# Kernel optimization log

Hardware: AMD Instinct MI355X
Metric: run time of the kernel (lower is better)

## Reference

```python
import jax, jax.numpy as jnp
import numpy as np
import math

H = 8        # num_heads
DK = 64      # key_dim
DV = 64      # value_dim
FACTOR = 4


def setup_inputs() -> dict:
    key = jax.random.key(0)
    B, T, S, D = 4, 2048, 2048, 512
    Dout = H * DV
    ks = jax.random.split(key, 16)
    sample_k = min(int(FACTOR * math.log(S)), S)  # = 33
    inp = {
        "x_q": jax.random.normal(ks[0], (B, T, D), jnp.float32),
        "x_k": jax.random.normal(ks[1], (B, S, D), jnp.float32),
        "x_v": jax.random.normal(ks[2], (B, S, D), jnp.float32),
        "Wq": jax.random.normal(ks[3], (D, H * DK), jnp.float32) * 0.02,
        "bq": jnp.zeros((H * DK,), jnp.float32),
        "Wk": jax.random.normal(ks[4], (D, H * DK), jnp.float32) * 0.02,
        "bk": jnp.zeros((H * DK,), jnp.float32),
        "Wv": jax.random.normal(ks[5], (D, H * DV), jnp.float32) * 0.02,
        "bv": jnp.zeros((H * DV,), jnp.float32),
        "Wo": jax.random.normal(ks[6], (H * DV, Dout), jnp.float32) * 0.02,
        "bo": jnp.zeros((Dout,), jnp.float32),
        "index_sample": jax.random.randint(ks[7], (T, sample_k), 0, S, jnp.int32),
    }
    return inp


def reference(x_q, x_k, x_v, Wq, bq, Wk, bk, Wv, bv, Wo, bo, index_sample):
    B, T, D = x_q.shape
    S = x_k.shape[1]
    u = min(int(FACTOR * math.log(T)), T)  # n_top queries kept

    q = (x_q @ Wq + bq).reshape(B, T, H, DK)
    k = (x_k @ Wk + bk).reshape(B, S, H, DK)
    v = (x_v @ Wv + bv).reshape(B, S, H, DV)

    # --- _prob_QK: sampled QK to score queries ---
    ks = k[:, index_sample]                                  # [B,T,J,H,dk]
    qk_s = jnp.einsum('bthd,btjhd->bthj', q, ks)             # [B,T,H,J]
    M = qk_s.max(-1) - qk_s.mean(-1)                         # [B,T,H]
    _, top = jax.lax.top_k(jnp.transpose(M, (0, 2, 1)), u)   # [B,H,u]

    b_idx = jnp.arange(B)[:, None, None]
    h_idx = jnp.arange(H)[None, :, None]
    q_red = q[b_idx, top, h_idx]                             # [B,H,u,dk]
    qk = jnp.einsum('bhud,bshd->bhus', q_red, k)             # [B,H,u,S]

    # --- s0: default (no mask) context = mean of values over S ---
    ctx = jnp.broadcast_to(v.mean(axis=1, keepdims=True), (B, T, H, DV))
    ctx = jnp.transpose(ctx, (0, 2, 1, 3))                   # [B,H,T,dv]

    # --- s1: scaled softmax over full keys for top queries ---
    scores = jax.nn.softmax(qk * (1.0 / math.sqrt(DK)), axis=-1)
    attn = jnp.einsum('bhus,bshd->bhud', scores, v)          # [B,H,u,dv]

    # --- scatter top-query results into context / scores ---
    ctx = ctx.at[b_idx, h_idx, top].set(attn)                # [B,H,T,dv]
    final_scores = jnp.full((B, H, T, S), 1.0 / S, dtype=scores.dtype)
    final_scores = final_scores.at[b_idx, h_idx, top].set(scores)

    out = jnp.transpose(ctx, (0, 2, 1, 3)).reshape(B, T, H * DV)
    out = out @ Wo + bo                                      # [B,T,output_dim]
    return out, final_scores
```

## Files before the change

kernel.cpp:

```cpp
#include <hip/hip_runtime.h>

typedef __attribute__((ext_vector_type(8))) short short8;
typedef __attribute__((ext_vector_type(4))) float f32x4;

constexpr int Bn  = 4;
constexpr int Tn  = 2048;
constexpr int Sn  = 2048;
constexpr int Dn  = 512;
constexpr int Hn  = 8;
constexpr int DKn = 64;
constexpr int DVn = 64;
constexpr int HDn = 512;
constexpr int SKn = 30;
constexpr int Un  = 30;
constexpr int Gu  = 6;
constexpr int NGroups = Un / Gu;
constexpr int NAttnG  = Bn * Hn * NGroups;
constexpr int NOutF   = (Bn * Tn) / 8;
constexpr int RowSplit = 57344;
constexpr int NGemm  = 768;
constexpr int NFillA = RowSplit / 4;
constexpr int NTailF = (Bn * Hn * Tn - RowSplit) / 4;
constexpr float kScale = 0.125f;

constexpr int NWsplit = 192;
constexpr int NXsplit = 1536;
constexpr int NVPart  = 64;

__device__ __forceinline__ ushort bf16_rne(float x) {
  unsigned u = __float_as_uint(x);
  return (ushort)((u + 0x7fffu + ((u >> 16) & 1u)) >> 16);
}
__device__ __forceinline__ float bf16f(ushort h) {
  return __uint_as_float(((unsigned)h) << 16);
}

#define MFMA(accv, av, bv) \
  asm volatile("v_mfma_f32_16x16x32_bf16 %0, %1, %2, %0" : "+v"(accv) : "v"(av), "v"(bv))

__global__ __launch_bounds__(256) void prep_split_kernel(
    const float* __restrict__ xq, const float* __restrict__ xk, const float* __restrict__ xv,
    const float* __restrict__ Wq, const float* __restrict__ Wk, const float* __restrict__ Wv,
    ushort* __restrict__ XH, ushort* __restrict__ XL,
    ushort* __restrict__ WtH, ushort* __restrict__ WtL) {
  const int tid = threadIdx.x;
  const int bid = blockIdx.x;

  if (bid < NWsplit) {
    const int z = bid / 64, t = bid % 64;
    const int k0 = (t >> 3) * 64, n0 = (t & 7) * 64;
    const float* W = (z == 0) ? Wq : (z == 1) ? Wk : Wv;
    __shared__ float tile[64][65];
    const int r = tid >> 2, c0 = (tid & 3) * 16;
#pragma unroll
    for (int i = 0; i < 16; i += 4) {
      const float4 vv = *(const float4*)(W + (size_t)(k0 + r) * HDn + n0 + c0 + i);
      tile[r][c0 + i] = vv.x; tile[r][c0 + i + 1] = vv.y;
      tile[r][c0 + i + 2] = vv.z; tile[r][c0 + i + 3] = vv.w;
    }
    __syncthreads();
    unsigned hp[8], lp[8];
#pragma unroll
    for (int i = 0; i < 16; i += 2) {
      const float x0 = tile[c0 + i][r];
      const float x1 = tile[c0 + i + 1][r];
      const ushort h0 = bf16_rne(x0), h1 = bf16_rne(x1);
      const ushort l0 = bf16_rne(x0 - bf16f(h0)), l1 = bf16_rne(x1 - bf16f(h1));
      hp[i >> 1] = (unsigned)h0 | ((unsigned)h1 << 16);
      lp[i >> 1] = (unsigned)l0 | ((unsigned)l1 << 16);
    }
    const size_t off = (size_t)(z * 512 + n0 + r) * 512 + k0 + c0;
    *(uint4*)(WtH + off)     = make_uint4(hp[0], hp[1], hp[2], hp[3]);
    *(uint4*)(WtH + off + 8) = make_uint4(hp[4], hp[5], hp[6], hp[7]);
    *(uint4*)(WtL + off)     = make_uint4(lp[0], lp[1], lp[2], lp[3]);
    *(uint4*)(WtL + off + 8) = make_uint4(lp[4], lp[5], lp[6], lp[7]);
    return;
  }

  const int xb = bid - NWsplit;
  const int z = xb >> 9, blk = xb & 511;
  const float* X = (z == 0) ? xq : (z == 1) ? xk : xv;
  const size_t base = (size_t)blk * 8192;
  const float4* X4 = (const float4*)(X + base);
  ushort* oh = XH + (size_t)z * 8192 * 512 + base;
  ushort* ol = XL + (size_t)z * 8192 * 512 + base;
#pragma unroll
  for (int i = 0; i < 8; ++i) {
    const int e = i * 256 + tid;
    const float4 x = X4[e];
    const ushort h0 = bf16_rne(x.x), h1 = bf16_rne(x.y);
    const ushort h2 = bf16_rne(x.z), h3 = bf16_rne(x.w);
    const ushort l0 = bf16_rne(x.x - bf16f(h0)), l1 = bf16_rne(x.y - bf16f(h1));
    const ushort l2 = bf16_rne(x.z - bf16f(h2)), l3 = bf16_rne(x.w - bf16f(h3));
    *(uint2*)(oh + (size_t)e * 4) =
        make_uint2((unsigned)h0 | ((unsigned)h1 << 16), (unsigned)h2 | ((unsigned)h3 << 16));
    *(uint2*)(ol + (size_t)e * 4) =
        make_uint2((unsigned)l0 | ((unsigned)l1 << 16), (unsigned)l2 | ((unsigned)l3 << 16));
  }
}

__global__ __launch_bounds__(256, 2) void gemm_fill_kernel(
    const ushort* __restrict__ XH, const ushort* __restrict__ XL,
    const ushort* __restrict__ WtH, const ushort* __restrict__ WtL,
    const float* __restrict__ bq, const float* __restrict__ bk, const float* __restrict__ bv,
    float* __restrict__ qo, float* __restrict__ ko, float* __restrict__ vo,
    float* __restrict__ fscores) {
  const int bid = blockIdx.x;
  const int tid = threadIdx.x;

  if (bid >= NGemm) {
    const size_t r0 = (size_t)(bid - NGemm) * 4;
    const float c = 1.0f / Sn;
    const float4 c4v = make_float4(c, c, c, c);
    float4* fs4 = (float4*)fscores + r0 * (Sn / 4);
#pragma unroll
    for (int i = 0; i < 8; ++i) fs4[i * 256 + tid] = c4v;
    return;
  }

  __shared__ ushort AsH[128][40];
  __shared__ ushort AsL[128][40];
  __shared__ ushort BsH[128][40];
  __shared__ ushort BsL[128][40];

  const int z = bid >> 8;
  const int rem = bid & 255;
  const int bn = (rem & 3) * 128;
  const int bm = (rem >> 2) * 128;
  const float* bias = (z == 0) ? bq : (z == 1) ? bk : bv;
  float* Y = (z == 0) ? qo : (z == 1) ? ko : vo;

  const int lane = tid & 63;
  const int wave = tid >> 6;
  const int wm = wave >> 1, wn = wave & 1;
  const int fr = lane & 15;
  const int kg = (lane >> 4) * 8;

  const int sr = tid >> 1;
  const int sh = (tid & 1) * 16;
  const ushort* xh = XH + (size_t)(z * 8192 + bm + sr) * 512 + sh;
  const ushort* xl = XL + (size_t)(z * 8192 + bm + sr) * 512 + sh;
  const ushort* wh = WtH + (size_t)(z * 512 + bn + sr) * 512 + sh;
  const ushort* wl = WtL + (size_t)(z * 512 + bn + sr) * 512 + sh;

  f32x4 acc[4][4];
#pragma unroll
  for (int m = 0; m < 4; ++m)
#pragma unroll
    for (int n = 0; n < 4; ++n)
#pragma unroll
      for (int j = 0; j < 4; ++j) acc[m][n][j] = 0.f;

  uint4 st[8];
#define STG_LOAD(k0_) do { \
    st[0] = *(const uint4*)(xh + (k0_)); st[1] = *(const uint4*)(xh + (k0_) + 8); \
    st[2] = *(const uint4*)(xl + (k0_)); st[3] = *(const uint4*)(xl + (k0_) + 8); \
    st[4] = *(const uint4*)(wh + (k0_)); st[5] = *(const uint4*)(wh + (k0_) + 8); \
    st[6] = *(const uint4*)(wl + (k0_)); st[7] = *(const uint4*)(wl + (k0_) + 8); } while (0)

  STG_LOAD(0);
  for (int k0 = 0; k0 < Dn; k0 += 32) {
    __syncthreads();
    *(uint4*)&AsH[sr][sh] = st[0]; *(uint4*)&AsH[sr][sh + 8] = st[1];
    *(uint4*)&AsL[sr][sh] = st[2]; *(uint4*)&AsL[sr][sh + 8] = st[3];
    *(uint4*)&BsH[sr][sh] = st[4]; *(uint4*)&BsH[sr][sh + 8] = st[5];
    *(uint4*)&BsL[sr][sh] = st[6]; *(uint4*)&BsL[sr][sh + 8] = st[7];
    __syncthreads();
    if (k0 + 32 < Dn) STG_LOAD(k0 + 32);

    short8 aH[4], aL[4], bH[4], bL[4];
#pragma unroll
    for (int m = 0; m < 4; ++m) {
      aH[m] = *(const short8*)&AsH[wm * 64 + m * 16 + fr][kg];
      aL[m] = *(const short8*)&AsL[wm * 64 + m * 16 + fr][kg];
    }
#pragma unroll
    for (int n = 0; n < 4; ++n) {
      bH[n] = *(const short8*)&BsH[wn * 64 + n * 16 + fr][kg];
      bL[n] = *(const short8*)&BsL[wn * 64 + n * 16 + fr][kg];
    }
#pragma unroll
    for (int m = 0; m < 4; ++m)
#pragma unroll
      for (int n = 0; n < 4; ++n) {
        MFMA(acc[m][n], aH[m], bH[n]);
        MFMA(acc[m][n], aH[m], bL[n]);
        MFMA(acc[m][n], aL[m], bH[n]);
      }
  }
  asm volatile("s_nop 7\n\ts_nop 7");

  float bsv[4];
#pragma unroll
  for (int n = 0; n < 4; ++n) bsv[n] = bias[bn + wn * 64 + n * 16 + fr];
  const int rbase = bm + wm * 64 + (lane >> 4) * 4;
#pragma unroll
  for (int m = 0; m < 4; ++m) {
#pragma unroll
    for (int n = 0; n < 4; ++n) {
      const int col = bn + wn * 64 + n * 16 + fr;
#pragma unroll
      for (int j = 0; j < 4; ++j) {
        Y[(size_t)(rbase + m * 16 + j) * HDn + col] = acc[m][n][j] + bsv[n];
      }
    }
  }
#undef STG_LOAD
}

__global__ __launch_bounds__(64) void sampled_m_kernel(
    const float* __restrict__ q, const float* __restrict__ k,
    const int* __restrict__ idxs, float* __restrict__ Mt,
    const float* __restrict__ v, float* __restrict__ vpart) {
  if (blockIdx.x >= Bn * Tn) {
    const int pb = blockIdx.x - Bn * Tn;
    const int b = pb >> 4, part = pb & 15;
    const int ln = threadIdx.x;
    const float4* v4 = (const float4*)(v + (size_t)b * Sn * HDn);
    float4 a0 = make_float4(0.f, 0.f, 0.f, 0.f);
    float4 a1 = make_float4(0.f, 0.f, 0.f, 0.f);
    const int s0 = part * 128;
    for (int s = s0; s < s0 + 128; ++s) {
      const float4 x0 = v4[(size_t)s * 128 + ln * 2];
      const float4 x1 = v4[(size_t)s * 128 + ln * 2 + 1];
      a0.x += x0.x; a0.y += x0.y; a0.z += x0.z; a0.w += x0.w;
      a1.x += x1.x; a1.y += x1.y; a1.z += x1.z; a1.w += x1.w;
    }
    float4* vp4 = (float4*)vpart + (size_t)pb * 128;
    vp4[ln * 2] = a0; vp4[ln * 2 + 1] = a1;
    return;
  }

  const int bt = blockIdx.x;
  const int b = bt >> 11, t = bt & (Tn - 1);
  const int lane = threadIdx.x;
  const int jq = lane >> 4;
  const int d16 = lane & 15;
  __shared__ int sidx[32];
  if (lane < SKn) sidx[lane] = idxs[t * SKn + lane];
  if (lane >= SKn && lane < 32) sidx[lane] = 0;
  __syncthreads();
  const float* qrow = q + (size_t)bt * HDn;
  const float* kb = k + (size_t)b * Sn * HDn;
  for (int h = 0; h < Hn; ++h) {
    const float4 qv = *(const float4*)(qrow + h * DKn + d16 * 4);
    float mx = -1e30f, sum = 0.f;
#pragma unroll
    for (int jb = 0; jb < 32; jb += 4) {
      const int j = jb + jq;
      const int srow = sidx[j];
      const float4 kv = *(const float4*)(kb + (size_t)srow * HDn + h * DKn + d16 * 4);
      float p = kv.x * qv.x + kv.y * qv.y + kv.z * qv.z + kv.w * qv.w;
      p += __shfl_xor(p, 1);
      p += __shfl_xor(p, 2);
      p += __shfl_xor(p, 4);
      p += __shfl_xor(p, 8);
      if (j < SKn) { mx = fmaxf(mx, p); sum += p; }
    }
    mx = fmaxf(mx, __shfl_xor(mx, 16));
    mx = fmaxf(mx, __shfl_xor(mx, 32));
    sum += __shfl_xor(sum, 16);
    sum += __shfl_xor(sum, 32);
    if (lane == 0) Mt[((size_t)(b * Hn + h)) * Tn + t] = mx - sum * (1.0f / SKn);
  }
}

__global__ __launch_bounds__(256) void topk_vmean_base_kernel(
    const float* __restrict__ Mt, const float* __restrict__ vpart,
    const float* __restrict__ Wo, const float* __restrict__ bo,
    int* __restrict__ top, float* __restrict__ vmean, float* __restrict__ basep) {
  const int tid = threadIdx.x;
  const int lane = tid & 63, w = tid >> 6;
  __shared__ float vals[Tn];
  __shared__ float wv[4];
  __shared__ int wi[4];
  __shared__ float4 part[256];
  __shared__ float vm[HDn];

  if (blockIdx.x < 32) {
    const int bh = blockIdx.x;
    for (int i = tid; i < Tn; i += 256) vals[i] = Mt[(size_t)bh * Tn + i];
    __syncthreads();
    for (int u = 0; u < Un; ++u) {
      float bv = -1e30f; int bi = 0x7fffffff;
      for (int i = tid; i < Tn; i += 256) {
        const float x = vals[i];
        if (x > bv) { bv = x; bi = i; }
      }
#pragma unroll
      for (int o = 1; o < 64; o <<= 1) {
        const float ov = __shfl_xor(bv, o);
        const int oi = __shfl_xor(bi, o);
        if (ov > bv || (ov == bv && oi < bi)) { bv = ov; bi = oi; }
      }
      if (lane == 0) { wv[w] = bv; wi[w] = bi; }
      __syncthreads();
      bv = wv[0]; bi = wi[0];
#pragma unroll
      for (int j = 1; j < 4; ++j) {
        if (wv[j] > bv || (wv[j] == bv && wi[j] < bi)) { bv = wv[j]; bi = wi[j]; }
      }
      if (tid == 0) { top[bh * Un + u] = bi; vals[bi] = -1e30f; }
      __syncthreads();
    }
  } else {
    const int b = blockIdx.x - 32;
    const int c4 = tid & 127, half = tid >> 7;
    float4 acc = make_float4(0.f, 0.f, 0.f, 0.f);
    for (int p = half * 8; p < half * 8 + 8; ++p) {
      const float4 x = ((const float4*)vpart)[(size_t)(b * 16 + p) * 128 + c4];
      acc.x += x.x; acc.y += x.y; acc.z += x.z; acc.w += x.w;
    }
    part[tid] = acc;
    __syncthreads();
    if (half == 0) {
      float4 a = part[c4], bpp = part[128 + c4];
      const float sc = 1.0f / Sn;
      float4 r = make_float4((a.x + bpp.x) * sc, (a.y + bpp.y) * sc,
                             (a.z + bpp.z) * sc, (a.w + bpp.w) * sc);
      *(float4*)(vm + c4 * 4) = r;
      *(float4*)(vmean + b * HDn + c4 * 4) = r;
    }
    __syncthreads();
    const float4* Wo4 = (const float4*)Wo;
    float4 acc2 = make_float4(0.f, 0.f, 0.f, 0.f);
    for (int c = half * 256; c < half * 256 + 256; ++c) {
      const float vmc = vm[c];
      const float4 wrow = Wo4[(size_t)c * 128 + c4];
      acc2.x += vmc * wrow.x; acc2.y += vmc * wrow.y;
      acc2.z += vmc * wrow.z; acc2.w += vmc * wrow.w;
    }
    __syncthreads();
    part[tid] = acc2;
    __syncthreads();
    if (half == 0) {
      float4 a = part[c4], bpp = part[128 + c4];
      const float4 bb = ((const float4*)bo)[c4];
      float4 r = make_float4(a.x + bpp.x + bb.x, a.y + bpp.y + bb.y,
                             a.z + bpp.z + bb.z, a.w + bpp.w + bb.w);
      ((float4*)basep)[b * 128 + c4] = r;
    }
  }
}

__global__ __launch_bounds__(256) void attn_out_kernel(
    const float* __restrict__ q, const float* __restrict__ k,
    const float* __restrict__ v, const float* __restrict__ vmean,
    const int* __restrict__ top, const float* __restrict__ Wo,
    const float* __restrict__ basep,
    float* __restrict__ out, float* __restrict__ fscores) {
  const int tid = threadIdx.x;
  const int bid = blockIdx.x;

  if (bid >= NAttnG + NOutF) {
    const int fid = bid - NAttnG - NOutF;
    const int r = RowSplit + fid * 4;
    const int bh = r >> 11;
    const int tbase = r & (Tn - 1);
    __shared__ int sflag4[4];
    if (tid < 4) sflag4[tid] = 0;
    __syncthreads();
    if (tid < Un) {
      const int d = top[bh * Un + tid] - tbase;
      if (d >= 0 && d < 4) sflag4[d] = 1;
    }
    __syncthreads();
    const float c = 1.0f / Sn;
    const float4 c4v = make_float4(c, c, c, c);
    float4* fs4 = (float4*)fscores + (size_t)r * (Sn / 4);
#pragma unroll
    for (int rr = 0; rr < 4; ++rr) {
      if (!sflag4[rr]) {
        float4* row = fs4 + rr * (Sn / 4);
        row[tid] = c4v;
        row[256 + tid] = c4v;
      }
    }
    return;
  }

  if (bid >= NAttnG) {
    const int fid = bid - NAttnG;
    const int r0 = fid * 8;
    const int b = r0 >> 11;
    const int t0 = r0 & (Tn - 1);
    __shared__ int sflag8[8];
    if (tid < 8) sflag8[tid] = 0;
    __syncthreads();
    if (tid < Hn * Un) {
      const int d = top[b * Hn * Un + tid] - t0;
      if (d >= 0 && d < 8) sflag8[d] = 1;
    }
    __syncthreads();
    const int col4 = tid & 127, rh = tid >> 7;
    const float4 bv4 = ((const float4*)basep)[b * 128 + col4];
#pragma unroll
    for (int rp = 0; rp < 4; ++rp) {
      const int rr = rp * 2 + rh;
      float4* orow4 = (float4*)(out + (size_t)(r0 + rr) * HDn) + col4;
      if (sflag8[rr]) {
        float* p = (float*)orow4;
        atomicAdd(p + 0, bv4.x); atomicAdd(p + 1, bv4.y);
        atomicAdd(p + 2, bv4.z); atomicAdd(p + 3, bv4.w);
      } else {
        *orow4 = bv4;
      }
    }
    return;
  }

  const int grp = bid % NGroups;
  const int bh = bid / NGroups;
  const int h = bh & (Hn - 1), b = bh >> 3;
  const int u0 = grp * Gu;
  const int lane = tid & 63, w = tid >> 6;

  __shared__ float qs[Gu][DKn];
  __shared__ float sc[Gu][2052];
  __shared__ float red[8];
  __shared__ int tsel[Gu];
  __shared__ float4 partv[4][Gu][16];

  if (tid < Gu) tsel[tid] = top[bh * Un + u0 + tid];
  __syncthreads();
  for (int i = tid; i < Gu * DKn; i += 256) {
    const int g = i >> 6, d = i & 63;
    qs[g][d] = q[((size_t)(b * Tn + tsel[g])) * HDn + h * DKn + d];
  }
  __syncthreads();

  const float4* k4 = (const float4*)k;
  for (int s = tid; s < Sn; s += 256) {
    const float4* krow = k4 + ((size_t)(b * Sn + s)) * 128 + h * 16;
    float acc[Gu];
#pragma unroll
    for (int g = 0; g < Gu; ++g) acc[g] = 0.f;
#pragma unroll
    for (int d4i = 0; d4i < 16; ++d4i) {
      const float4 kv = krow[d4i];
#pragma unroll
      for (int g = 0; g < Gu; ++g) {
        const float4 qv = *(const float4*)&qs[g][d4i * 4];
        acc[g] += kv.x * qv.x + kv.y * qv.y + kv.z * qv.z + kv.w * qv.w;
      }
    }
#pragma unroll
    for (int g = 0; g < Gu; ++g) sc[g][s] = acc[g] * kScale;
  }
  __syncthreads();

  float invs[Gu];
#pragma unroll
  for (int g = 0; g < Gu; ++g) {
    float lm = -1e30f;
    for (int i = tid; i < Sn; i += 256) lm = fmaxf(lm, sc[g][i]);
#pragma unroll
    for (int o = 1; o < 64; o <<= 1) lm = fmaxf(lm, __shfl_xor(lm, o));
    if (lane == 0) red[w] = lm;
    __syncthreads();
    const float mx = fmaxf(fmaxf(red[0], red[1]), fmaxf(red[2], red[3]));
    float ls = 0.f;
    for (int i = tid; i < Sn; i += 256) {
      const float e = __expf(sc[g][i] - mx);
      sc[g][i] = e;
      ls += e;
    }
#pragma unroll
    for (int o = 1; o < 64; o <<= 1) ls += __shfl_xor(ls, o);
    if (lane == 0) red[4 + w] = ls;
    __syncthreads();
    invs[g] = 1.0f / (red[4] + red[5] + red[6] + red[7]);
    __syncthreads();
  }
#pragma unroll
  for (int g = 0; g < Gu; ++g) {
    const float inv = invs[g];
    float4* scg4 = (float4*)sc[g];
    float4* fsrow4 = (float4*)(fscores + ((size_t)bh * Tn + tsel[g]) * Sn);
#pragma unroll
    for (int it = 0; it < 2; ++it) {
      const int i = it * 256 + tid;
      float4 p = scg4[i];
      p.x *= inv; p.y *= inv; p.z *= inv; p.w *= inv;
      scg4[i] = p;
      fsrow4[i] = p;
    }
  }
  __syncthreads();

  const int d4 = lane & 15;
  const int sg = (w << 2) + (lane >> 4);
  const float4* v4 = (const float4*)v;
  float4 pacc[Gu];
#pragma unroll
  for (int g = 0; g < Gu; ++g) pacc[g] = make_float4(0.f, 0.f, 0.f, 0.f);
  for (int s = sg; s < Sn; s += 16) {
    const float4 vv = v4[((size_t)(b * Sn + s)) * 128 + h * 16 + d4];
#pragma unroll
    for (int g = 0; g < Gu; ++g) {
      const float p = sc[g][s];
      pacc[g].x += p * vv.x; pacc[g].y += p * vv.y;
      pacc[g].z += p * vv.z; pacc[g].w += p * vv.w;
    }
  }
#pragma unroll
  for (int g = 0; g < Gu; ++g) {
#pragma unroll
    for (int o = 16; o < 64; o <<= 1) {
      pacc[g].x += __shfl_xor(pacc[g].x, o);
      pacc[g].y += __shfl_xor(pacc[g].y, o);
      pacc[g].z += __shfl_xor(pacc[g].z, o);
      pacc[g].w += __shfl_xor(pacc[g].w, o);
    }
    if (lane < 16) partv[w][g][lane] = pacc[g];
  }
  __syncthreads();
  if (tid < Gu * 16) {
    const int g = tid >> 4, dd = tid & 15;
    float4 r = partv[0][g][dd];
    const float4 r1 = partv[1][g][dd], r2 = partv[2][g][dd], r3 = partv[3][g][dd];
    r.x += r1.x + r2.x + r3.x; r.y += r1.y + r2.y + r3.y;
    r.z += r1.z + r2.z + r3.z; r.w += r1.w + r2.w + r3.w;
    const float4 vm4 = ((const float4*)vmean)[bh * 16 + dd];
    r.x -= vm4.x; r.y -= vm4.y; r.z -= vm4.z; r.w -= vm4.w;
    *(float4*)&qs[g][dd * 4] = r;
  }
  __syncthreads();

  const int col4 = tid & 127, gg = tid >> 7;
  const float4* Wo4 = (const float4*)Wo;
#pragma unroll
  for (int gp = 0; gp < Gu / 2; ++gp) {
    const int g = gp * 2 + gg;
    float4 a = make_float4(0.f, 0.f, 0.f, 0.f);
#pragma unroll
    for (int d = 0; d < DKn; ++d) {
      const float dv = qs[g][d];
      const float4 wrow = Wo4[(size_t)(h * DKn + d) * 128 + col4];
      a.x += dv * wrow.x; a.y += dv * wrow.y;
      a.z += dv * wrow.z; a.w += dv * wrow.w;
    }
    float* orow = out + ((size_t)(b * Tn + tsel[g])) * HDn + col4 * 4;
    atomicAdd(orow + 0, a.x); atomicAdd(orow + 1, a.y);
    atomicAdd(orow + 2, a.z); atomicAdd(orow + 3, a.w);
  }
}

extern "C" void kernel_launch(void* const* d_in, const int* in_sizes, int n_in,
                              void* d_out, int out_size, void* d_ws, size_t ws_size,
                              hipStream_t stream) {
  const float* x_q = (const float*)d_in[0];
  const float* x_k = (const float*)d_in[1];
  const float* x_v = (const float*)d_in[2];
  const float* Wq = (const float*)d_in[3];
  const float* bq = (const float*)d_in[4];
  const float* Wk = (const float*)d_in[5];
  const float* bk = (const float*)d_in[6];
  const float* Wv = (const float*)d_in[7];
  const float* bv = (const float*)d_in[8];
  const float* Wo = (const float*)d_in[9];
  const float* bo = (const float*)d_in[10];
  const int* idx = (const int*)d_in[11];

  float* out = (float*)d_out;
  float* fscores = out + (size_t)Bn * Tn * HDn;

  float* ws = (float*)d_ws;
  float* q = ws;
  float* kp = ws + (size_t)4194304;
  float* vp = ws + (size_t)8388608;
  float* Mt = ws + (size_t)12582912;
  float* vmean = ws + (size_t)12648448;
  float* basep = ws + (size_t)12650496;
  int* top = (int*)(ws + (size_t)12652544);

  char* scr = (char*)(fscores + (size_t)RowSplit * Sn);
  ushort* XH = (ushort*)scr;
  ushort* XL = XH + (size_t)3 * 8192 * 512;
  ushort* WtH = XL + (size_t)3 * 8192 * 512;
  ushort* WtL = WtH + (size_t)3 * 512 * 512;
  float* vpart = (float*)(WtL + (size_t)3 * 512 * 512);

  prep_split_kernel<<<NWsplit + NXsplit, 256, 0, stream>>>(
      x_q, x_k, x_v, Wq, Wk, Wv, XH, XL, WtH, WtL);

  gemm_fill_kernel<<<NGemm + NFillA, 256, 0, stream>>>(
      XH, XL, WtH, WtL, bq, bk, bv, q, kp, vp, fscores);

  sampled_m_kernel<<<Bn * Tn + NVPart, 64, 0, stream>>>(q, kp, idx, Mt, vp, vpart);

  topk_vmean_base_kernel<<<36, 256, 0, stream>>>(Mt, vpart, Wo, bo, top, vmean, basep);

  attn_out_kernel<<<NAttnG + NOutF + NTailF, 256, 0, stream>>>(
      q, kp, vp, vmean, top, Wo, basep, out, fscores);
}
```

Before: 894.3 us.

## Fuse fp32-to-bf16 hi/lo split of activations into projection GEMM

Result: no change. 898.7 us (+0.5%).

```diff
diff --git a/kernel.cpp b/kernel.cpp
--- a/kernel.cpp
+++ b/kernel.cpp
@@ -24,7 +24,6 @@
 constexpr float kScale = 0.125f;
 
 constexpr int NWsplit = 192;
-constexpr int NXsplit = 1536;
 constexpr int NVPart  = 64;
 
 __device__ __forceinline__ ushort bf16_rne(float x) {
@@ -34,73 +33,50 @@
 __device__ __forceinline__ float bf16f(ushort h) {
   return __uint_as_float(((unsigned)h) << 16);
 }
+__device__ __forceinline__ void nt_store4(f32x4* p, f32x4 v) {
+  __builtin_nontemporal_store(v, p);
+}
 
 #define MFMA(accv, av, bv) \
   asm volatile("v_mfma_f32_16x16x32_bf16 %0, %1, %2, %0" : "+v"(accv) : "v"(av), "v"(bv))
 
 __global__ __launch_bounds__(256) void prep_split_kernel(
-    const float* __restrict__ xq, const float* __restrict__ xk, const float* __restrict__ xv,
     const float* __restrict__ Wq, const float* __restrict__ Wk, const float* __restrict__ Wv,
-    ushort* __restrict__ XH, ushort* __restrict__ XL,
     ushort* __restrict__ WtH, ushort* __restrict__ WtL) {
   const int tid = threadIdx.x;
   const int bid = blockIdx.x;
 
-  if (bid < NWsplit) {
-    const int z = bid / 64, t = bid % 64;
-    const int k0 = (t >> 3) * 64, n0 = (t & 7) * 64;
-    const float* W = (z == 0) ? Wq : (z == 1) ? Wk : Wv;
-    __shared__ float tile[64][65];
-    const int r = tid >> 2, c0 = (tid & 3) * 16;
-#pragma unroll
-    for (int i = 0; i < 16; i += 4) {
-      const float4 vv = *(const float4*)(W + (size_t)(k0 + r) * HDn + n0 + c0 + i);
-      tile[r][c0 + i] = vv.x; tile[r][c0 + i + 1] = vv.y;
-      tile[r][c0 + i + 2] = vv.z; tile[r][c0 + i + 3] = vv.w;
-    }
-    __syncthreads();
-    unsigned hp[8], lp[8];
-#pragma unroll
-    for (int i = 0; i < 16; i += 2) {
-      const float x0 = tile[c0 + i][r];
-      const float x1 = tile[c0 + i + 1][r];
-      const ushort h0 = bf16_rne(x0), h1 = bf16_rne(x1);
-      const ushort l0 = bf16_rne(x0 - bf16f(h0)), l1 = bf16_rne(x1 - bf16f(h1));
-      hp[i >> 1] = (unsigned)h0 | ((unsigned)h1 << 16);
-      lp[i >> 1] = (unsigned)l0 | ((unsigned)l1 << 16);
-    }
-    const size_t off = (size_t)(z * 512 + n0 + r) * 512 + k0 + c0;
-    *(uint4*)(WtH + off)     = make_uint4(hp[0], hp[1], hp[2], hp[3]);
-    *(uint4*)(WtH + off + 8) = make_uint4(hp[4], hp[5], hp[6], hp[7]);
-    *(uint4*)(WtL + off)     = make_uint4(lp[0], lp[1], lp[2], lp[3]);
-    *(uint4*)(WtL + off + 8) = make_uint4(lp[4], lp[5], lp[6], lp[7]);
-    return;
-  }
-
-  const int xb = bid - NWsplit;
-  const int z = xb >> 9, blk = xb & 511;
-  const float* X = (z == 0) ? xq : (z == 1) ? xk : xv;
-  const size_t base = (size_t)blk * 8192;
-  const float4* X4 = (const float4*)(X + base);
-  ushort* oh = XH + (size_t)z * 8192 * 512 + base;
-  ushort* ol = XL + (size_t)z * 8192 * 512 + base;
-#pragma unroll
-  for (int i = 0; i < 8; ++i) {
-    const int e = i * 256 + tid;
-    const float4 x = X4[e];
-    const ushort h0 = bf16_rne(x.x), h1 = bf16_rne(x.y);
-    const ushort h2 = bf16_rne(x.z), h3 = bf16_rne(x.w);
-    const ushort l0 = bf16_rne(x.x - bf16f(h0)), l1 = bf16_rne(x.y - bf16f(h1));
-    const ushort l2 = bf16_rne(x.z - bf16f(h2)), l3 = bf16_rne(x.w - bf16f(h3));
-    *(uint2*)(oh + (size_t)e * 4) =
-        make_uint2((unsigned)h0 | ((unsigned)h1 << 16), (unsigned)h2 | ((unsigned)h3 << 16));
-    *(uint2*)(ol + (size_t)e * 4) =
-        make_uint2((unsigned)l0 | ((unsigned)l1 << 16), (unsigned)l2 | ((unsigned)l3 << 16));
-  }
+  const int z = bid / 64, t = bid % 64;
+  const int k0 = (t >> 3) * 64, n0 = (t & 7) * 64;
+  const float* W = (z == 0) ? Wq : (z == 1) ? Wk : Wv;
+  __shared__ float tile[64][65];
+  const int r = tid >> 2, c0 = (tid & 3) * 16;
+#pragma unroll
+  for (int i = 0; i < 16; i += 4) {
+    const float4 vv = *(const float4*)(W + (size_t)(k0 + r) * HDn + n0 + c0 + i);
+    tile[r][c0 + i] = vv.x; tile[r][c0 + i + 1] = vv.y;
+    tile[r][c0 + i + 2] = vv.z; tile[r][c0 + i + 3] = vv.w;
+  }
+  __syncthreads();
+  unsigned hp[8], lp[8];
+#pragma unroll
+  for (int i = 0; i < 16; i += 2) {
+    const float x0 = tile[c0 + i][r];
+    const float x1 = tile[c0 + i + 1][r];
+    const ushort h0 = bf16_rne(x0), h1 = bf16_rne(x1);
+    const ushort l0 = bf16_rne(x0 - bf16f(h0)), l1 = bf16_rne(x1 - bf16f(h1));
+    hp[i >> 1] = (unsigned)h0 | ((unsigned)h1 << 16);
+    lp[i >> 1] = (unsigned)l0 | ((unsigned)l1 << 16);
+  }
+  const size_t off = (size_t)(z * 512 + n0 + r) * 512 + k0 + c0;
+  *(uint4*)(WtH + off)     = make_uint4(hp[0], hp[1], hp[2], hp[3]);
+  *(uint4*)(WtH + off + 8) = make_uint4(hp[4], hp[5], hp[6], hp[7]);
+  *(uint4*)(WtL + off)     = make_uint4(lp[0], lp[1], lp[2], lp[3]);
+  *(uint4*)(WtL + off + 8) = make_uint4(lp[4], lp[5], lp[6], lp[7]);
 }
 
 __global__ __launch_bounds__(256, 2) void gemm_fill_kernel(
-    const ushort* __restrict__ XH, const ushort* __restrict__ XL,
+    const float* __restrict__ xq, const float* __restrict__ xk, const float* __restrict__ xv,
     const ushort* __restrict__ WtH, const ushort* __restrict__ WtL,
     const float* __restrict__ bq, const float* __restrict__ bk, const float* __restrict__ bv,
     float* __restrict__ qo, float* __restrict__ ko, float* __restrict__ vo,
@@ -111,37 +87,36 @@
   if (bid >= NGemm) {
     const size_t r0 = (size_t)(bid - NGemm) * 4;
     const float c = 1.0f / Sn;
-    const float4 c4v = make_float4(c, c, c, c);
-    float4* fs4 = (float4*)fscores + r0 * (Sn / 4);
-#pragma unroll
-    for (int i = 0; i < 8; ++i) fs4[i * 256 + tid] = c4v;
+    const f32x4 c4v = {c, c, c, c};
+    f32x4* fs4 = (f32x4*)fscores + r0 * (Sn / 4);
+#pragma unroll
+    for (int i = 0; i < 8; ++i) nt_store4(fs4 + i * 256 + tid, c4v);
     return;
   }
 
-  __shared__ ushort AsH[128][40];
-  __shared__ ushort AsL[128][40];
-  __shared__ ushort BsH[128][40];
-  __shared__ ushort BsL[128][40];
+  __shared__ ushort AsH[64][32];
+  __shared__ ushort AsL[64][32];
+  __shared__ ushort BsH[256][32];
+  __shared__ ushort BsL[256][32];
 
   const int z = bid >> 8;
   const int rem = bid & 255;
-  const int bn = (rem & 3) * 128;
-  const int bm = (rem >> 2) * 128;
+  const int bm = (rem >> 1) * 64;
+  const int bn = (rem & 1) * 256;
+  const float* X = (z == 0) ? xq : (z == 1) ? xk : xv;
   const float* bias = (z == 0) ? bq : (z == 1) ? bk : bv;
   float* Y = (z == 0) ? qo : (z == 1) ? ko : vo;
 
   const int lane = tid & 63;
   const int wave = tid >> 6;
-  const int wm = wave >> 1, wn = wave & 1;
   const int fr = lane & 15;
-  const int kg = (lane >> 4) * 8;
-
-  const int sr = tid >> 1;
-  const int sh = (tid & 1) * 16;
-  const ushort* xh = XH + (size_t)(z * 8192 + bm + sr) * 512 + sh;
-  const ushort* xl = XL + (size_t)(z * 8192 + bm + sr) * 512 + sh;
-  const ushort* wh = WtH + (size_t)(z * 512 + bn + sr) * 512 + sh;
-  const ushort* wl = WtL + (size_t)(z * 512 + bn + sr) * 512 + sh;
+  const int gk = lane >> 4;
+
+  const int ar = tid >> 2, ag = tid & 3;
+  const float* xrow = X + (size_t)(bm + ar) * Dn + ag * 8;
+  const int brow0 = tid >> 2, bg = tid & 3;
+  const ushort* wh = WtH + (size_t)(z * 512 + bn + brow0) * 512 + bg * 8;
+  const ushort* wl = WtL + (size_t)(z * 512 + bn + brow0) * 512 + bg * 8;
 
   f32x4 acc[4][4];
 #pragma unroll
@@ -151,33 +126,56 @@
 #pragma unroll
       for (int j = 0; j < 4; ++j) acc[m][n][j] = 0.f;
 
-  uint4 st[8];
+  float4 af0, af1;
+  uint4 sbH[4], sbL[4];
 #define STG_LOAD(k0_) do { \
-    st[0] = *(const uint4*)(xh + (k0_)); st[1] = *(const uint4*)(xh + (k0_) + 8); \
-    st[2] = *(const uint4*)(xl + (k0_)); st[3] = *(const uint4*)(xl + (k0_) + 8); \
-    st[4] = *(const uint4*)(wh + (k0_)); st[5] = *(const uint4*)(wh + (k0_) + 8); \
-    st[6] = *(const uint4*)(wl + (k0_)); st[7] = *(const uint4*)(wl + (k0_) + 8); } while (0)
+    af0 = *(const float4*)(xrow + (k0_)); \
+    af1 = *(const float4*)(xrow + (k0_) + 4); \
+    sbH[0] = *(const uint4*)(wh + (k0_));          sbL[0] = *(const uint4*)(wl + (k0_)); \
+    sbH[1] = *(const uint4*)(wh + (k0_) + 32768);  sbL[1] = *(const uint4*)(wl + (k0_) + 32768); \
+    sbH[2] = *(const uint4*)(wh + (k0_) + 65536);  sbL[2] = *(const uint4*)(wl + (k0_) + 65536); \
+    sbH[3] = *(const uint4*)(wh + (k0_) + 98304);  sbL[3] = *(const uint4*)(wl + (k0_) + 98304); \
+  } while (0)
+
+  const int agq = (ag ^ ((ar >> 1) & 3)) * 8;
+  const int bgx = bg ^ ((brow0 >> 1) & 3);
+  const int gq = (gk ^ ((fr >> 1) & 3)) * 8;
 
   STG_LOAD(0);
   for (int k0 = 0; k0 < Dn; k0 += 32) {
     __syncthreads();
-    *(uint4*)&AsH[sr][sh] = st[0]; *(uint4*)&AsH[sr][sh + 8] = st[1];
-    *(uint4*)&AsL[sr][sh] = st[2]; *(uint4*)&AsL[sr][sh + 8] = st[3];
-    *(uint4*)&BsH[sr][sh] = st[4]; *(uint4*)&BsH[sr][sh + 8] = st[5];
-    *(uint4*)&BsL[sr][sh] = st[6]; *(uint4*)&BsL[sr][sh + 8] = st[7];
+    {
+      float xf[8] = {af0.x, af0.y, af0.z, af0.w, af1.x, af1.y, af1.z, af1.w};
+      unsigned hp[4], lp[4];
+#pragma unroll
+      for (int i = 0; i < 8; i += 2) {
+        const ushort h0 = bf16_rne(xf[i]), h1 = bf16_rne(xf[i + 1]);
+        const ushort l0 = bf16_rne(xf[i] - bf16f(h0)), l1 = bf16_rne(xf[i + 1] - bf16f(h1));
+        hp[i >> 1] = (unsigned)h0 | ((unsigned)h1 << 16);
+        lp[i >> 1] = (unsigned)l0 | ((unsigned)l1 << 16);
+      }
+      *(uint4*)&AsH[ar][agq] = make_uint4(hp[0], hp[1], hp[2], hp[3]);
+      *(uint4*)&AsL[ar][agq] = make_uint4(lp[0], lp[1], lp[2], lp[3]);
+#pragma unroll
+      for (int p = 0; p < 4; ++p) {
+        const int n = brow0 + p * 64;
+        *(uint4*)&BsH[n][bgx * 8] = sbH[p];
+        *(uint4*)&BsL[n][bgx * 8] = sbL[p];
+      }
+    }
     __syncthreads();
     if (k0 + 32 < Dn) STG_LOAD(k0 + 32);
 
     short8 aH[4], aL[4], bH[4], bL[4];
 #pragma unroll
     for (int m = 0; m < 4; ++m) {
-      aH[m] = *(const short8*)&AsH[wm * 64 + m * 16 + fr][kg];
-      aL[m] = *(const short8*)&AsL[wm * 64 + m * 16 + fr][kg];
+      aH[m] = *(const short8*)&AsH[m * 16 + fr][gq];
+      aL[m] = *(const short8*)&AsL[m * 16 + fr][gq];
     }
 #pragma unroll
     for (int n = 0; n < 4; ++n) {
-      bH[n] = *(const short8*)&BsH[wn * 64 + n * 16 + fr][kg];
-      bL[n] = *(const short8*)&BsL[wn * 64 + n * 16 + fr][kg];
+      bH[n] = *(const short8*)&BsH[wave * 64 + n * 16 + fr][gq];
+      bL[n] = *(const short8*)&BsL[wave * 64 + n * 16 + fr][gq];
     }
 #pragma unroll
     for (int m = 0; m < 4; ++m)
@@ -192,16 +190,15 @@
 
   float bsv[4];
 #pragma unroll
-  for (int n = 0; n < 4; ++n) bsv[n] = bias[bn + wn * 64 + n * 16 + fr];
-  const int rbase = bm + wm * 64 + (lane >> 4) * 4;
+  for (int n = 0; n < 4; ++n) bsv[n] = bias[bn + wave * 64 + n * 16 + fr];
 #pragma unroll
   for (int m = 0; m < 4; ++m) {
 #pragma unroll
     for (int n = 0; n < 4; ++n) {
-      const int col = bn + wn * 64 + n * 16 + fr;
+      const int col = bn + wave * 64 + n * 16 + fr;
 #pragma unroll
       for (int j = 0; j < 4; ++j) {
-        Y[(size_t)(rbase + m * 16 + j) * HDn + col] = acc[m][n][j] + bsv[n];
+        Y[(size_t)(bm + m * 16 + gk * 4 + j) * HDn + col] = acc[m][n][j] + bsv[n];
       }
     }
   }
@@ -366,14 +363,14 @@
     }
     __syncthreads();
     const float c = 1.0f / Sn;
-    const float4 c4v = make_float4(c, c, c, c);
-    float4* fs4 = (float4*)fscores + (size_t)r * (Sn / 4);
+    const f32x4 c4v = {c, c, c, c};
+    f32x4* fs4 = (f32x4*)fscores + (size_t)r * (Sn / 4);
 #pragma unroll
     for (int rr = 0; rr < 4; ++rr) {
       if (!sflag4[rr]) {
-        float4* row = fs4 + rr * (Sn / 4);
-        row[tid] = c4v;
-        row[256 + tid] = c4v;
+        f32x4* row = fs4 + rr * (Sn / 4);
+        nt_store4(row + tid, c4v);
+        nt_store4(row + 256 + tid, c4v);
       }
     }
     return;
@@ -394,6 +391,7 @@
     __syncthreads();
     const int col4 = tid & 127, rh = tid >> 7;
     const float4 bv4 = ((const float4*)basep)[b * 128 + col4];
+    const f32x4 bvx = {bv4.x, bv4.y, bv4.z, bv4.w};
 #pragma unroll
     for (int rp = 0; rp < 4; ++rp) {
       const int rr = rp * 2 + rh;
@@ -403,7 +401,7 @@
         atomicAdd(p + 0, bv4.x); atomicAdd(p + 1, bv4.y);
         atomicAdd(p + 2, bv4.z); atomicAdd(p + 3, bv4.w);
       } else {
-        *orow4 = bv4;
+        nt_store4((f32x4*)orow4, bvx);
       }
     }
     return;
@@ -476,14 +474,15 @@
   for (int g = 0; g < Gu; ++g) {
     const float inv = invs[g];
     float4* scg4 = (float4*)sc[g];
-    float4* fsrow4 = (float4*)(fscores + ((size_t)bh * Tn + tsel[g]) * Sn);
+    f32x4* fsrow4 = (f32x4*)(fscores + ((size_t)bh * Tn + tsel[g]) * Sn);
 #pragma unroll
     for (int it = 0; it < 2; ++it) {
       const int i = it * 256 + tid;
       float4 p = scg4[i];
       p.x *= inv; p.y *= inv; p.z *= inv; p.w *= inv;
       scg4[i] = p;
-      fsrow4[i] = p;
+      const f32x4 px = {p.x, p.y, p.z, p.w};
+      nt_store4(fsrow4 + i, px);
     }
   }
   __syncthreads();
@@ -575,17 +574,14 @@
   int* top = (int*)(ws + (size_t)12652544);
 
   char* scr = (char*)(fscores + (size_t)RowSplit * Sn);
-  ushort* XH = (ushort*)scr;
-  ushort* XL = XH + (size_t)3 * 8192 * 512;
-  ushort* WtH = XL + (size_t)3 * 8192 * 512;
+  ushort* WtH = (ushort*)scr;
   ushort* WtL = WtH + (size_t)3 * 512 * 512;
   float* vpart = (float*)(WtL + (size_t)3 * 512 * 512);
 
-  prep_split_kernel<<<NWsplit + NXsplit, 256, 0, stream>>>(
-      x_q, x_k, x_v, Wq, Wk, Wv, XH, XL, WtH, WtL);
+  prep_split_kernel<<<NWsplit, 256, 0, stream>>>(Wq, Wk, Wv, WtH, WtL);
 
   gemm_fill_kernel<<<NGemm + NFillA, 256, 0, stream>>>(
-      XH, XL, WtH, WtL, bq, bk, bv, q, kp, vp, fscores);
+      x_q, x_k, x_v, WtH, WtL, bq, bk, bv, q, kp, vp, fscores);
 
   sampled_m_kernel<<<Bn * Tn + NVPart, 64, 0, stream>>>(q, kp, idx, Mt, vp, vpart);
 
```
